# Performance work log

Hardware: AMD Instinct MI355X
Metric: run time of the kernel (lower is better)

Reference implementation:

```python
import jax, jax.numpy as jnp
import numpy as np

BINS = 50            # init kwarg
SCALING = (-1.0, 1.0)  # init kwarg
EPS = 1e-6


def setup_inputs() -> dict:
    key = jax.random.key(0)
    X = jax.random.normal(key, (256, 6, 128), dtype=jnp.float32)
    return {"X": X}


def reference(X) -> jnp.ndarray:
    lo, hi = SCALING
    W = X.shape[-1]
    lead = X.shape[:-1]

    # --- minmax_scaler: scale last dim into [lo, hi] ---
    X_min = X.min(axis=-1, keepdims=True)
    X_max = X.max(axis=-1, keepdims=True)
    X_scaled = (X - X_min) / (X_max - X_min + EPS) * (hi - lo) + lo

    # --- bucketize: torch.bucketize(right=False) == searchsorted side='left' ---
    boundaries = jnp.linspace(lo, hi, BINS + 1)[1:-1]  # (bins-1,) inner edges
    n_bins = boundaries.shape[0] + 1                   # == BINS
    binned = jnp.searchsorted(boundaries, X_scaled, side='left')  # int, same shape as X

    bflat = binned.reshape(-1, W)      # (S, W), S = prod(lead)
    S = bflat.shape[0]

    # --- mtm_compute: per-series transition histogram via scatter-add ---
    idx = bflat[:, :-1] * n_bins + bflat[:, 1:]        # (S, W-1) flat (i->j) indices
    mtm = jnp.zeros((S, n_bins * n_bins), dtype=X.dtype)
    mtm = mtm.at[jnp.arange(S)[:, None], idx].add(jnp.ones_like(idx, dtype=X.dtype))
    mtm = mtm.reshape(S, n_bins, n_bins)
    row_sum = mtm.sum(axis=-1, keepdims=True)          # (S, n_bins, 1)
    mtm = mtm / jnp.where(row_sum == 0, 1.0, row_sum)  # row-normalize, guard empty rows

    # --- final gather: MTF[t1, t2] = mtm[bin(t1), bin(t2)] ---
    mtm_flat = mtm.reshape(S, n_bins * n_bins)
    gidx = (n_bins * bflat[:, :, None] + bflat[:, None, :]).reshape(S, W * W)
    mtf = jnp.take_along_axis(mtm_flat, gidx, axis=1)  # (S, W*W)
    return mtf.reshape(lead + (W, W))
```

## Files before the change

kernel.cpp:

```cpp
#include <hip/hip_runtime.h>
#include <float.h>

#define W  128
#define NB 50

__global__ __launch_bounds__(256) void mtf_kernel(const float* __restrict__ X,
                                                  float* __restrict__ out) {
    __shared__ int   bins[W];
    __shared__ int   hist[NB * NB];
    __shared__ int   rowsum[NB];
    __shared__ float probs[NB * NB];
    __shared__ float redmin[4], redmax[4];

    const int tid = threadIdx.x;
    const int s   = blockIdx.x;
    const float* xrow = X + (size_t)s * W;

    float v = 0.0f;
    float vmin = FLT_MAX, vmax = -FLT_MAX;
    if (tid < W) { v = xrow[tid]; vmin = v; vmax = v; }
    #pragma unroll
    for (int off = 32; off >= 1; off >>= 1) {
        vmin = fminf(vmin, __shfl_down(vmin, off, 64));
        vmax = fmaxf(vmax, __shfl_down(vmax, off, 64));
    }
    if ((tid & 63) == 0) { redmin[tid >> 6] = vmin; redmax[tid >> 6] = vmax; }

    for (int i = tid; i < NB * NB; i += 256) hist[i] = 0;
    if (tid < NB) rowsum[tid] = 0;
    __syncthreads();

    const float mn = fminf(fminf(redmin[0], redmin[1]), fminf(redmin[2], redmin[3]));
    const float mx = fmaxf(fmaxf(redmax[0], redmax[1]), fmaxf(redmax[2], redmax[3]));
    const float d  = (mx - mn) + 1e-6f;

    if (tid < W) {
        float q   = (v - mn) / d;
        float xsc = q * 2.0f - 1.0f;
        double xd = (double)xsc;
        int b = 0;
        #pragma unroll
        for (int k = 1; k <= NB - 1; ++k) {
            double bk = -1.0 + 0.04 * (double)k;
            b += (bk < xd) ? 1 : 0;
        }
        bins[tid] = b;
    }
    __syncthreads();

    if (tid < W - 1) {
        int bi = bins[tid], bj = bins[tid + 1];
        atomicAdd(&hist[bi * NB + bj], 1);
        atomicAdd(&rowsum[bi], 1);
    }
    __syncthreads();

    for (int i = tid; i < NB * NB; i += 256) {
        int rs = rowsum[i / NB];
        probs[i] = (float)hist[i] / (float)(rs == 0 ? 1 : rs);
    }
    __syncthreads();

    float* orow = out + (size_t)s * W * W;
    const int wv   = tid >> 6;
    const int lane = tid & 63;
    const int c4   = (lane & 31) * 4;
    const int half = lane >> 5;
    const int b0 = bins[c4], b1 = bins[c4 + 1], b2 = bins[c4 + 2], b3 = bins[c4 + 3];
    #pragma unroll
    for (int it = 0; it < 16; ++it) {
        int row = (wv << 5) + (it << 1) + half;
        int rb  = bins[row] * NB;
        float4 o;
        o.x = probs[rb + b0];
        o.y = probs[rb + b1];
        o.z = probs[rb + b2];
        o.w = probs[rb + b3];
        *(float4*)(orow + row * W + c4) = o;
    }
}

extern "C" void kernel_launch(void* const* d_in, const int* in_sizes, int n_in,
                              void* d_out, int out_size, void* d_ws, size_t ws_size,
                              hipStream_t stream) {
    const float* X = (const float*)d_in[0];
    float* out = (float*)d_out;
    int S = in_sizes[0] / W;
    mtf_kernel<<<dim3(S), dim3(256), 0, stream>>>(X, out);
}
```

Measured before the change: 105.1 us.

## Split MTF into stats kernel and expand kernel via workspace

Splits the fused kernel into two launches. The first computes the bins and the normalized transition matrix per series and writes them to workspace. The second loads them back and expands them into the 128x128 output. The aim is probably to shrink the LDS and register footprint of each kernel so more blocks fit per CU, but it adds a second launch and a global round-trip of about 10KB per series. It falls back to the fused kernel when the workspace is too small.

```diff
diff --git a/kernel.cpp b/kernel.cpp
--- a/kernel.cpp
+++ b/kernel.cpp
@@ -3,6 +3,100 @@
 
 #define W  128
 #define NB 50
+#define PROBS_F (NB * NB)
+
+__global__ __launch_bounds__(256) void mtf_stats(const float* __restrict__ X,
+                                                 float* __restrict__ wprobs,
+                                                 int*   __restrict__ wbins) {
+    __shared__ int   bins[W];
+    __shared__ int   hist[NB * NB];
+    __shared__ int   rowsum[NB];
+    __shared__ float redmin[4], redmax[4];
+
+    const int tid = threadIdx.x;
+    const int s   = blockIdx.x;
+    const float* xrow = X + (size_t)s * W;
+
+    float v = 0.0f;
+    float vmin = FLT_MAX, vmax = -FLT_MAX;
+    if (tid < W) { v = xrow[tid]; vmin = v; vmax = v; }
+    #pragma unroll
+    for (int off = 32; off >= 1; off >>= 1) {
+        vmin = fminf(vmin, __shfl_down(vmin, off, 64));
+        vmax = fmaxf(vmax, __shfl_down(vmax, off, 64));
+    }
+    if ((tid & 63) == 0) { redmin[tid >> 6] = vmin; redmax[tid >> 6] = vmax; }
+
+    for (int i = tid; i < NB * NB; i += 256) hist[i] = 0;
+    if (tid < NB) rowsum[tid] = 0;
+    __syncthreads();
+
+    const float mn = fminf(fminf(redmin[0], redmin[1]), fminf(redmin[2], redmin[3]));
+    const float mx = fmaxf(fmaxf(redmax[0], redmax[1]), fmaxf(redmax[2], redmax[3]));
+    const float d  = (mx - mn) + 1e-6f;
+
+    if (tid < W) {
+        float q   = (v - mn) / d;
+        float xsc = q * 2.0f - 1.0f;
+        double xd = (double)xsc;
+        int b = 0;
+        #pragma unroll
+        for (int k = 1; k <= NB - 1; ++k) {
+            double bk = -1.0 + 0.04 * (double)k;
+            b += (bk < xd) ? 1 : 0;
+        }
+        bins[tid] = b;
+        wbins[(size_t)s * W + tid] = b;
+    }
+    __syncthreads();
+
+    if (tid < W - 1) {
+        int bi = bins[tid], bj = bins[tid + 1];
+        atomicAdd(&hist[bi * NB + bj], 1);
+        atomicAdd(&rowsum[bi], 1);
+    }
+    __syncthreads();
+
+    float* po = wprobs + (size_t)s * PROBS_F;
+    for (int i = tid; i < NB * NB; i += 256) {
+        int rs = rowsum[i / NB];
+        po[i] = (float)hist[i] / (float)(rs == 0 ? 1 : rs);
+    }
+}
+
+__global__ __launch_bounds__(256) void mtf_expand(const float* __restrict__ wprobs,
+                                                  const int*   __restrict__ wbins,
+                                                  float* __restrict__ out) {
+    __shared__ __align__(16) float probs[NB * NB];
+    __shared__ __align__(16) int   bins[W];
+
+    const int tid = threadIdx.x;
+    const int s   = blockIdx.x;
+
+    const float4* ps = (const float4*)(wprobs + (size_t)s * PROBS_F);
+    #pragma unroll
+    for (int i = tid; i < PROBS_F / 4; i += 256) ((float4*)probs)[i] = ps[i];
+    if (tid < W / 4) ((int4*)bins)[tid] = ((const int4*)(wbins + (size_t)s * W))[tid];
+    __syncthreads();
+
+    float* orow = out + (size_t)s * W * W;
+    const int wv   = tid >> 6;
+    const int lane = tid & 63;
+    const int c4   = (lane & 31) * 4;
+    const int half = lane >> 5;
+    const int b0 = bins[c4], b1 = bins[c4 + 1], b2 = bins[c4 + 2], b3 = bins[c4 + 3];
+    #pragma unroll
+    for (int it = 0; it < 16; ++it) {
+        int row = (wv << 5) + (it << 1) + half;
+        int rb  = bins[row] * NB;
+        float4 o;
+        o.x = probs[rb + b0];
+        o.y = probs[rb + b1];
+        o.z = probs[rb + b2];
+        o.w = probs[rb + b3];
+        *(float4*)(orow + row * W + c4) = o;
+    }
+}
 
 __global__ __launch_bounds__(256) void mtf_kernel(const float* __restrict__ X,
                                                   float* __restrict__ out) {
@@ -86,5 +180,16 @@
     const float* X = (const float*)d_in[0];
     float* out = (float*)d_out;
     int S = in_sizes[0] / W;
-    mtf_kernel<<<dim3(S), dim3(256), 0, stream>>>(X, out);
+
+    const size_t probs_bytes = (size_t)S * PROBS_F * sizeof(float);
+    const size_t bins_bytes  = (size_t)S * W * sizeof(int);
+
+    if (d_ws && ws_size >= probs_bytes + bins_bytes) {
+        float* wprobs = (float*)d_ws;
+        int*   wbins  = (int*)((char*)d_ws + probs_bytes);
+        mtf_stats <<<dim3(S), dim3(256), 0, stream>>>(X, wprobs, wbins);
+        mtf_expand<<<dim3(S), dim3(256), 0, stream>>>(wprobs, wbins, out);
+    } else {
+        mtf_kernel<<<dim3(S), dim3(256), 0, stream>>>(X, out);
+    }
 }
```

After: 115.7 us. 1.1x slower.
